# Kernel optimization log

Measured on AMD Instinct MI355X. Metric: run time of the kernel, lower is better.

Reference implementation:

```python
import jax, jax.numpy as jnp
import numpy as np

NUM_HEADS = 16
NUM_UNITS = 1024
NEG = -2.0**32 + 1.0
EPS = 1e-8


def setup_inputs() -> dict:
    key = jax.random.key(0)
    ks = jax.random.split(key, 8)
    B, T, C = 2, 2048, 1024
    U = NUM_UNITS
    x = jax.random.normal(ks[0], (B, T, C), dtype=jnp.float32)
    s = 1.0 / np.sqrt(C)
    Wq = jax.random.normal(ks[1], (C, U), dtype=jnp.float32) * s
    Wk = jax.random.normal(ks[2], (C, U), dtype=jnp.float32) * s
    Wv = jax.random.normal(ks[3], (C, U), dtype=jnp.float32) * s
    bq = jnp.zeros((U,), dtype=jnp.float32)
    bk = jnp.zeros((U,), dtype=jnp.float32)
    bv = jnp.zeros((U,), dtype=jnp.float32)
    gamma = jnp.ones((U,), dtype=jnp.float32)
    beta = jnp.zeros((U,), dtype=jnp.float32)
    return {"x": x, "Wq": Wq, "bq": bq, "Wk": Wk, "bk": bk,
            "Wv": Wv, "bv": bv, "gamma": gamma, "beta": beta}


def _attention(x, Wq, bq, Wk, bk, Wv, bv, gamma, beta):
    B, T, C = x.shape
    H = NUM_HEADS
    U = NUM_UNITS
    dh = U // H
    # Dense projections with relu activation (Keras Dense(activation='relu'))
    Q = jax.nn.relu(x @ Wq + bq)  # [B, T, U]
    K = jax.nn.relu(x @ Wk + bk)
    V = jax.nn.relu(x @ Wv + bv)
    # split into heads: tf.split(axis=2) + concat(axis=0) == [B, T, H, dh]
    Qh = Q.reshape(B, T, H, dh)
    Kh = K.reshape(B, T, H, dh)
    Vh = V.reshape(B, T, H, dh)
    # scaled dot-product scores: scale by sqrt(d_head) (K_ last dim after split)
    scores = jnp.einsum('bqhd,bkhd->bhqk', Qh, Kh) / np.sqrt(dh)
    # key mask: sign(|sum(keys, -1)|) over the ORIGINAL keys input (= x)
    key_mask = jnp.sign(jnp.abs(jnp.sum(x, axis=-1)))  # [B, Tk]
    scores = jnp.where(key_mask[:, None, None, :] == 0, NEG, scores)
    # causal mask (lower-triangular)
    tril = jnp.tril(jnp.ones((T, T), dtype=scores.dtype))
    scores = jnp.where(tril[None, None, :, :] == 0, NEG, scores)
    attn = jax.nn.softmax(scores, axis=-1)
    # query mask: multiply attention rows for zero queries
    query_mask = jnp.sign(jnp.abs(jnp.sum(x, axis=-1)))  # [B, Tq]
    attn = attn * query_mask[:, None, :, None]
    # dropout rate is 0 -> identity
    out = jnp.einsum('bhqk,bkhd->bqhd', attn, Vh).reshape(B, T, U)
    # residual with original queries
    out = out + x
    # layer norm over last axis (tf.nn.moments: biased variance)
    mean = jnp.mean(out, axis=-1, keepdims=True)
    var = jnp.mean((out - mean) ** 2, axis=-1, keepdims=True)
    normalized = (out - mean) / jnp.sqrt(var + EPS)
    return gamma * normalized + beta


def reference(x, Wq, bq, Wk, bk, Wv, bv, gamma, beta):
    return _attention(x, Wq, bq, Wk, bk, Wv, bv, gamma, beta)
```

## Files before the change

kernel.cpp:

```cpp
#include <hip/hip_runtime.h>
#include <math.h>

#define BB 2
#define TT 2048
#define CC 1024
#define UU 1024
#define HH 16
#define DH 64
#define BT (BB*TT)

typedef __attribute__((ext_vector_type(8))) __bf16 bf16x8;
typedef __attribute__((ext_vector_type(4))) __bf16 bf16x4;
typedef __attribute__((ext_vector_type(4))) float f32x4;

#define GLL16(g, l) __builtin_amdgcn_global_load_lds( \
    (__attribute__((address_space(1))) const void*)(g), \
    (__attribute__((address_space(3))) void*)(l), 16, 0, 0)

#define C2EXP 0.18033688011112042f
#define MBIAS 64.0f

__global__ __launch_bounds__(256) void prep_kernel(
    const float* __restrict__ x, float* __restrict__ kadd, __bf16* __restrict__ xb,
    const float* __restrict__ Wq, const float* __restrict__ Wk,
    const float* __restrict__ Wv, __bf16* __restrict__ Wt) {
    const int bx = blockIdx.x;
    const int t = threadIdx.x;
    if (bx < BT) {
        int row = bx;
        float4 v = *(const float4*)&x[(size_t)row * CC + t * 4];
        bf16x4 o;
        o[0] = (__bf16)v.x; o[1] = (__bf16)v.y; o[2] = (__bf16)v.z; o[3] = (__bf16)v.w;
        *(bf16x4*)&xb[(size_t)row * CC + t * 4] = o;
        float s = v.x + v.y + v.z + v.w;
#pragma unroll
        for (int off = 32; off; off >>= 1) s += __shfl_down(s, off, 64);
        __shared__ float red[4];
        int lane = t & 63, w = t >> 6;
        if (lane == 0) red[w] = s;
        __syncthreads();
        if (t == 0) {
            float tot = red[0] + red[1] + red[2] + red[3];
            kadd[row] = (tot == 0.f ? -1.0e30f : 0.f) - MBIAS;
        }
    } else {
        int bz = bx - BT;
        int z = bz >> 8, rem = bz & 255;
        const float* W = z == 0 ? Wq : (z == 1 ? Wk : Wv);
        __bf16* Out = Wt + (size_t)z * CC * UU;
        __shared__ float tile[64][65];
        int n0 = (rem & 15) * 64, k0 = (rem >> 4) * 64;
        int r = t >> 4, c4 = (t & 15) * 4;
#pragma unroll
        for (int i = 0; i < 4; ++i) {
            float4 v = *(const float4*)&W[(size_t)(k0 + r + i * 16) * UU + n0 + c4];
            tile[r + i * 16][c4 + 0] = v.x; tile[r + i * 16][c4 + 1] = v.y;
            tile[r + i * 16][c4 + 2] = v.z; tile[r + i * 16][c4 + 3] = v.w;
        }
        __syncthreads();
#pragma unroll
        for (int i = 0; i < 4; ++i) {
            int nr = r + i * 16;
            bf16x4 o;
            o[0] = (__bf16)tile[c4 + 0][nr]; o[1] = (__bf16)tile[c4 + 1][nr];
            o[2] = (__bf16)tile[c4 + 2][nr]; o[3] = (__bf16)tile[c4 + 3][nr];
            *(bf16x4*)&Out[(size_t)(n0 + nr) * CC + k0 + c4] = o;
        }
    }
}

__global__ __launch_bounds__(256, 4) void qkv_mfma(
    const __bf16* __restrict__ xb, const __bf16* __restrict__ Wt_all,
    const float* __restrict__ bq, const float* __restrict__ bk,
    const float* __restrict__ bv,
    __bf16* __restrict__ Qo, __bf16* __restrict__ Ko, __bf16* __restrict__ VTo) {
    const int z = blockIdx.z;
    const __bf16* Wt = Wt_all + (size_t)z * CC * UU;
    const float* bias = z == 0 ? bq : (z == 1 ? bk : bv);

    const int n0 = blockIdx.x * 128, m0 = blockIdx.y * 128;
    const int t = threadIdx.x, w = t >> 6, lane = t & 63;
    const int quad = lane >> 4, nn = lane & 15;
    const int wr = w >> 1, wc = w & 1;

    __shared__ __bf16 smem[2 * 128 * 64];
    __bf16* As = smem;
    __bf16* Bs = smem + 128 * 64;

    f32x4 acc[4][4];
#pragma unroll
    for (int i = 0; i < 4; ++i)
#pragma unroll
        for (int j = 0; j < 4; ++j) acc[i][j] = (f32x4){0.f, 0.f, 0.f, 0.f};

    for (int k0 = 0; k0 < CC; k0 += 64) {
        __syncthreads();
#pragma unroll
        for (int i = 0; i < 4; ++i) {
            int c = i * 256 + t;
            int row = c >> 3;
            int gc = ((c & 7) ^ (row & 7)) * 8;
            GLL16(&xb[(size_t)(m0 + row) * CC + k0 + gc], &As[c * 8]);
            GLL16(&Wt[(size_t)(n0 + row) * CC + k0 + gc], &Bs[c * 8]);
        }
        __syncthreads();
#pragma unroll
        for (int kk = 0; kk < 2; ++kk) {
            bf16x8 af[4], bfr[4];
#pragma unroll
            for (int i = 0; i < 4; ++i) {
                int R = wr * 64 + i * 16 + nn;
                af[i] = *(const bf16x8*)&As[R * 64 + (((kk * 4 + quad) ^ (R & 7)) * 8)];
            }
#pragma unroll
            for (int j = 0; j < 4; ++j) {
                int R = wc * 64 + j * 16 + nn;
                bfr[j] = *(const bf16x8*)&Bs[R * 64 + (((kk * 4 + quad) ^ (R & 7)) * 8)];
            }
#pragma unroll
            for (int i = 0; i < 4; ++i)
#pragma unroll
                for (int j = 0; j < 4; ++j)
                    acc[i][j] = __builtin_amdgcn_mfma_f32_16x16x32_bf16(af[i], bfr[j], acc[i][j], 0, 0, 0);
        }
    }

    __bf16* cw = &smem[w * 1024];
    float bv4[4];
#pragma unroll
    for (int j = 0; j < 4; ++j) bv4[j] = bias[n0 + wc * 64 + j * 16 + nn];

    if (z < 2) {
        __bf16* Out = z == 0 ? Qo : Ko;
#pragma unroll
        for (int i = 0; i < 4; ++i) {
            __syncthreads();
#pragma unroll
            for (int j = 0; j < 4; ++j)
#pragma unroll
                for (int r = 0; r < 4; ++r)
                    cw[(quad * 4 + r) * 64 + j * 16 + nn] =
                        (__bf16)fmaxf(acc[i][j][r] + bv4[j], 0.f);
            __syncthreads();
            int rr = lane >> 2, cc = (lane & 3) * 16;
            bf16x8 v0 = *(const bf16x8*)&cw[rr * 64 + cc];
            bf16x8 v1 = *(const bf16x8*)&cw[rr * 64 + cc + 8];
            size_t o = (size_t)(m0 + wr * 64 + i * 16 + rr) * UU + n0 + wc * 64 + cc;
            *(bf16x8*)&Out[o] = v0;
            *(bf16x8*)&Out[o + 8] = v1;
        }
    } else {
#pragma unroll
        for (int i = 0; i < 4; ++i) {
            __syncthreads();
#pragma unroll
            for (int j = 0; j < 4; ++j)
#pragma unroll
                for (int r = 0; r < 4; ++r)
                    cw[(j * 16 + nn) * 16 + quad * 4 + r] =
                        (__bf16)fmaxf(acc[i][j][r] + bv4[j], 0.f);
            __syncthreads();
            bf16x8 v0 = *(const bf16x8*)&cw[lane * 16];
            bf16x8 v1 = *(const bf16x8*)&cw[lane * 16 + 8];
            size_t o = (size_t)(n0 + wc * 64 + lane) * BT + m0 + wr * 64 + i * 16;
            *(bf16x8*)&VTo[o] = v0;
            *(bf16x8*)&VTo[o + 8] = v1;
        }
    }
}

__global__ __launch_bounds__(256, 4) void attn_mfma(
    const __bf16* __restrict__ Q, const __bf16* __restrict__ K,
    const __bf16* __restrict__ Vt, const float* __restrict__ kadd,
    float* __restrict__ Op0, float* __restrict__ Op1,
    float* __restrict__ lq0, float* __restrict__ lq1) {
    const int cx = blockIdx.x;
    const int bh = blockIdx.y, b = bh >> 4, h = bh & 15;
    int qt, kst, ket, slot;
    if (cx < 16) { qt = cx; kst = 0; ket = qt; slot = 0; }
    else {
        int q2 = (cx - 16) >> 1;
        qt = 16 + q2;
        int len0 = (qt + 2) >> 1;
        slot = (cx - 16) & 1;
        if (slot) { kst = len0; ket = qt; }
        else      { kst = 0;    ket = len0 - 1; }
    }
    const int col0 = h * 64, rowbase = b * TT, q0 = qt * 64;
    const bool hasdiag = (ket == qt);

    const int t = threadIdx.x;
    const int w = t >> 6, lane = t & 63, quad = lane >> 4, nn = lane & 15;
    const int s7 = nn & 7;

    __shared__ __align__(16) __bf16 ks[2][64 * 64];
    __shared__ __align__(16) __bf16 vt[2][64 * 64];
    __shared__ __align__(16) __bf16 ps[64 * 64];

    const int c0 = t;
    const int r0 = c0 >> 3, g0 = ((c0 & 7) ^ (r0 & 7)) * 8;
    const int prow = 16 * w + nn;
    const int qg = q0 + prow;

    const __bf16* kp0 = &K[(size_t)(rowbase + kst * 64 + r0) * UU + col0 + g0];
    const __bf16* kp1 = kp0 + 32 * (size_t)UU;
    const __bf16* vp0 = &Vt[(size_t)(col0 + r0) * BT + rowbase + kst * 64 + g0];
    const __bf16* vp1 = vp0 + 32 * (size_t)BT;
    const float* kap = &kadd[rowbase + kst * 64 + quad * 4];

    f32x4 ka[4];
#pragma unroll
    for (int ct = 0; ct < 4; ++ct) ka[ct] = *(const f32x4*)&kap[ct * 16];
    kap += 64;
    const __bf16* qrow = &Q[(size_t)(rowbase + qg) * UU + col0];
    bf16x8 bq0 = *(const bf16x8*)&qrow[quad * 8];
    bf16x8 bq1 = *(const bf16x8*)&qrow[32 + quad * 8];

    GLL16(kp0, &ks[0][c0 * 8]);
    GLL16(kp1, &ks[0][c0 * 8 + 2048]);
    GLL16(vp0, &vt[0][c0 * 8]);
    GLL16(vp1, &vt[0][c0 * 8 + 2048]);
    kp0 += 64 * (size_t)UU; kp1 += 64 * (size_t)UU;
    vp0 += 64; vp1 += 64;
    asm volatile("s_waitcnt vmcnt(0)" ::: "memory");
    __builtin_amdgcn_s_barrier();

    float lp = 0.f;
    f32x4 oc[4];
#pragma unroll
    for (int dt = 0; dt < 4; ++dt) oc[dt] = (f32x4){0.f, 0.f, 0.f, 0.f};

#define ATTN_CORE(KSC, VTC, DIAG)                                              \
  {                                                                            \
    const __bf16* ksc = (KSC);                                                 \
    const __bf16* vtc = (VTC);                                                 \
    _Pragma("unroll")                                                          \
    for (int ct = 0; ct < 4; ++ct) {                                           \
      int krow = ct * 16 + nn;                                                 \
      bf16x8 a0 = *(const bf16x8*)&ksc[krow * 64 + ((quad ^ s7) * 8)];         \
      bf16x8 a1 = *(const bf16x8*)&ksc[krow * 64 + (((4 + quad) ^ s7) * 8)];   \
      f32x4 sc = (f32x4){0.f, 0.f, 0.f, 0.f};                                  \
      sc = __builtin_amdgcn_mfma_f32_16x16x32_bf16(a0, bq0, sc, 0, 0, 0);      \
      sc = __builtin_amdgcn_mfma_f32_16x16x32_bf16(a1, bq1, sc, 0, 0, 0);      \
      bf16x4 pw;                                                               \
      _Pragma("unroll")                                                        \
      for (int r = 0; r < 4; ++r) {                                            \
        float arg = fmaf(sc[r], C2EXP, ka[ct][r]);                             \
        if (DIAG) {                                                            \
          int kl = ct * 16 + quad * 4 + r;                                     \
          if (kl > prow) arg = -1.0e30f;                                       \
        }                                                                      \
        float p = __builtin_amdgcn_exp2f(arg);                                 \
        lp += p;                                                               \
        pw[r] = (__bf16)p;                                                     \
      }                                                                        \
      int chunk = ct * 2 + (quad >> 1);                                        \
      *(bf16x4*)&ps[prow * 64 + ((chunk ^ s7) * 8) + (quad & 1) * 4] = pw;     \
    }                                                                          \
    bf16x8 bp0 = *(const bf16x8*)&ps[prow * 64 + ((quad ^ s7) * 8)];           \
    bf16x8 bp1 = *(const bf16x8*)&ps[prow * 64 + (((4 + quad) ^ s7) * 8)];     \
    _Pragma("unroll")                                                          \
    for (int dt = 0; dt < 4; ++dt) {                                           \
      int vrow = dt * 16 + nn;                                                 \
      bf16x8 a0 = *(const bf16x8*)&vtc[vrow * 64 + ((quad ^ s7) * 8)];         \
      bf16x8 a1 = *(const bf16x8*)&vtc[vrow * 64 + (((4 + quad) ^ s7) * 8)];   \
      oc[dt] = __builtin_amdgcn_mfma_f32_16x16x32_bf16(a0, bp0, oc[dt], 0, 0, 0); \
      oc[dt] = __builtin_amdgcn_mfma_f32_16x16x32_bf16(a1, bp1, oc[dt], 0, 0, 0); \
    }                                                                          \
  }

    int cur = 0;
    for (int kt = kst; kt < ket; ++kt) {
        f32x4 kan[4];
#pragma unroll
        for (int ct = 0; ct < 4; ++ct) kan[ct] = *(const f32x4*)&kap[ct * 16];
        kap += 64;
        GLL16(kp0, &ks[cur ^ 1][c0 * 8]);
        GLL16(kp1, &ks[cur ^ 1][c0 * 8 + 2048]);
        GLL16(vp0, &vt[cur ^ 1][c0 * 8]);
        GLL16(vp1, &vt[cur ^ 1][c0 * 8 + 2048]);
        kp0 += 64 * (size_t)UU; kp1 += 64 * (size_t)UU;
        vp0 += 64; vp1 += 64;
        ATTN_CORE(ks[cur], vt[cur], false)
#pragma unroll
        for (int ct = 0; ct < 4; ++ct) ka[ct] = kan[ct];
        cur ^= 1;
        asm volatile("s_waitcnt vmcnt(0)" ::: "memory");
        __builtin_amdgcn_s_barrier();
    }
    if (hasdiag) {
        ATTN_CORE(ks[cur], vt[cur], true)
    } else {
        ATTN_CORE(ks[cur], vt[cur], false)
    }
#undef ATTN_CORE

    float l = lp;
    l += __shfl_xor(l, 16, 64);
    l += __shfl_xor(l, 32, 64);
    const int grow = rowbase + qg;
    float* Op;
    size_t orow;
    if (slot) { Op = Op1; orow = (size_t)(grow - (b + 1) * 1024); }
    else      { Op = Op0; orow = (size_t)grow; }
    if (quad == 0) (slot ? lq1 : lq0)[(size_t)grow * HH + h] = l;
#pragma unroll
    for (int dt = 0; dt < 4; ++dt)
        *(f32x4*)&Op[orow * UU + col0 + dt * 16 + quad * 4] = oc[dt];
}

__global__ __launch_bounds__(256) void ln_kernel(
    const float* __restrict__ Op0, const float* __restrict__ Op1,
    const float* __restrict__ lq0, const float* __restrict__ lq1,
    const float* __restrict__ kadd, const float* __restrict__ x,
    const float* __restrict__ gamma, const float* __restrict__ beta,
    float* __restrict__ out) {
    int row = blockIdx.x;
    int b = row >> 11;
    int qt = (row & (TT - 1)) >> 6;
    size_t base = (size_t)row * UU;
    int t = threadIdx.x;
    int h = t >> 4;
    float l = lq0[(size_t)row * HH + h];
    f32x4 o = *(const f32x4*)&Op0[base + t * 4];
    if (qt >= 16) {
        l += lq1[(size_t)row * HH + h];
        size_t base1 = (size_t)(row - (b + 1) * 1024) * UU;
        f32x4 o1 = *(const f32x4*)&Op1[base1 + t * 4];
        o[0] += o1[0]; o[1] += o1[1]; o[2] += o1[2]; o[3] += o1[3];
    }
    float qsel = (kadd[row] < -1.0e29f) ? 0.f : 1.f;
    float mult = qsel / fmaxf(l, 1e-37f);
    float4 xv = *(const float4*)&x[base + t * 4];
    float v0 = o[0] * mult + xv.x, v1 = o[1] * mult + xv.y;
    float v2 = o[2] * mult + xv.z, v3 = o[3] * mult + xv.w;
    float s1 = v0 + v1 + v2 + v3;
    float s2 = v0 * v0 + v1 * v1 + v2 * v2 + v3 * v3;
#pragma unroll
    for (int off = 32; off; off >>= 1) {
        s1 += __shfl_down(s1, off, 64);
        s2 += __shfl_down(s2, off, 64);
    }
    __shared__ float r1[4], r2[4];
    int lane = t & 63, w = t >> 6;
    if (lane == 0) { r1[w] = s1; r2[w] = s2; }
    __syncthreads();
    s1 = r1[0] + r1[1] + r1[2] + r1[3];
    s2 = r2[0] + r2[1] + r2[2] + r2[3];
    float mean = s1 * (1.0f / 1024.0f);
    float var = s2 * (1.0f / 1024.0f) - mean * mean;
    float rstd = rsqrtf(var + 1e-8f);
    float4 g = *(const float4*)&gamma[t * 4];
    float4 be = *(const float4*)&beta[t * 4];
    float4 ores;
    ores.x = g.x * (v0 - mean) * rstd + be.x;
    ores.y = g.y * (v1 - mean) * rstd + be.y;
    ores.z = g.z * (v2 - mean) * rstd + be.z;
    ores.w = g.w * (v3 - mean) * rstd + be.w;
    *(float4*)&out[base + t * 4] = ores;
}

extern "C" void kernel_launch(void* const* d_in, const int* in_sizes, int n_in,
                              void* d_out, int out_size, void* d_ws, size_t ws_size,
                              hipStream_t stream) {
    const float* x     = (const float*)d_in[0];
    const float* Wq    = (const float*)d_in[1];
    const float* bq    = (const float*)d_in[2];
    const float* Wk    = (const float*)d_in[3];
    const float* bk    = (const float*)d_in[4];
    const float* Wv    = (const float*)d_in[5];
    const float* bv    = (const float*)d_in[6];
    const float* gamma = (const float*)d_in[7];
    const float* beta  = (const float*)d_in[8];
    float* out = (float*)d_out;

    char* wsb = (char*)d_ws;
    const size_t MB = 1024ull * 1024;
    __bf16* xb = (__bf16*)(wsb);
    __bf16* Wt = (__bf16*)(wsb + 8 * MB);
    float* Op0 = (float*)(wsb);
    __bf16* Qb = (__bf16*)(wsb + 16 * MB);
    __bf16* Kb = (__bf16*)(wsb + 24 * MB);
    __bf16* Vt = (__bf16*)(wsb + 32 * MB);
    float* kadd = (float*)(wsb + 40 * MB);
    float* Op1  = (float*)(wsb + 41 * MB);
    float* lq0  = (float*)(wsb + 49 * MB);
    float* lq1  = (float*)(wsb + 50 * MB);

    prep_kernel<<<dim3(BT + 768), dim3(256), 0, stream>>>(x, kadd, xb, Wq, Wk, Wv, Wt);
    qkv_mfma<<<dim3(UU / 128, BT / 128, 3), dim3(256), 0, stream>>>(
        xb, Wt, bq, bk, bv, Qb, Kb, Vt);
    attn_mfma<<<dim3(48, BB * HH), dim3(256), 0, stream>>>(
        Qb, Kb, Vt, kadd, Op0, Op1, lq0, lq1);
    ln_kernel<<<dim3(BT), dim3(256), 0, stream>>>(
        Op0, Op1, lq0, lq1, kadd, x, gamma, beta, out);
}
```

Before: 180.6 us.

## Pair light and heavy causal query tiles per block for balanced attention work

Changes the causal attention work split. Before, each block took one query tile, and the longer tiles were split in two. Now each of 32 blocks per head pairs query tile p with tile 31-p, with the two halves of the key range covering the pair's combined work, so every block does about 17 key tiles. The short tiles are finished in place and written already normalized as bf16, which lets the layer-norm kernel skip reading partial sums and row totals for those rows. The cost is a more complex control flow with a shared LDS double buffer carried across the two tiles, and reduced precision in the stored attention output for half the rows.

```diff
diff --git a/kernel.cpp b/kernel.cpp
--- a/kernel.cpp
+++ b/kernel.cpp
@@ -172,22 +172,13 @@
 __global__ __launch_bounds__(256, 4) void attn_mfma(
     const __bf16* __restrict__ Q, const __bf16* __restrict__ K,
     const __bf16* __restrict__ Vt, const float* __restrict__ kadd,
-    float* __restrict__ Op0, float* __restrict__ Op1,
+    __bf16* __restrict__ Obf, float* __restrict__ Op0, float* __restrict__ Op1,
     float* __restrict__ lq0, float* __restrict__ lq1) {
     const int cx = blockIdx.x;
+    const int p = cx >> 1, half = cx & 1;
     const int bh = blockIdx.y, b = bh >> 4, h = bh & 15;
-    int qt, kst, ket, slot;
-    if (cx < 16) { qt = cx; kst = 0; ket = qt; slot = 0; }
-    else {
-        int q2 = (cx - 16) >> 1;
-        qt = 16 + q2;
-        int len0 = (qt + 2) >> 1;
-        slot = (cx - 16) & 1;
-        if (slot) { kst = len0; ket = qt; }
-        else      { kst = 0;    ket = len0 - 1; }
-    }
-    const int col0 = h * 64, rowbase = b * TT, q0 = qt * 64;
-    const bool hasdiag = (ket == qt);
+    const int col0 = h * 64, rowbase = b * TT;
+    const int qa = p, qb = 31 - p;
 
     const int t = threadIdx.x;
     const int w = t >> 6, lane = t & 63, quad = lane >> 4, nn = lane & 15;
@@ -200,35 +191,27 @@
     const int c0 = t;
     const int r0 = c0 >> 3, g0 = ((c0 & 7) ^ (r0 & 7)) * 8;
     const int prow = 16 * w + nn;
-    const int qg = q0 + prow;
-
-    const __bf16* kp0 = &K[(size_t)(rowbase + kst * 64 + r0) * UU + col0 + g0];
-    const __bf16* kp1 = kp0 + 32 * (size_t)UU;
-    const __bf16* vp0 = &Vt[(size_t)(col0 + r0) * BT + rowbase + kst * 64 + g0];
-    const __bf16* vp1 = vp0 + 32 * (size_t)BT;
-    const float* kap = &kadd[rowbase + kst * 64 + quad * 4];
-
-    f32x4 ka[4];
-#pragma unroll
-    for (int ct = 0; ct < 4; ++ct) ka[ct] = *(const f32x4*)&kap[ct * 16];
-    kap += 64;
-    const __bf16* qrow = &Q[(size_t)(rowbase + qg) * UU + col0];
-    bf16x8 bq0 = *(const bf16x8*)&qrow[quad * 8];
-    bf16x8 bq1 = *(const bf16x8*)&qrow[32 + quad * 8];
-
-    GLL16(kp0, &ks[0][c0 * 8]);
-    GLL16(kp1, &ks[0][c0 * 8 + 2048]);
-    GLL16(vp0, &vt[0][c0 * 8]);
-    GLL16(vp1, &vt[0][c0 * 8 + 2048]);
-    kp0 += 64 * (size_t)UU; kp1 += 64 * (size_t)UU;
-    vp0 += 64; vp1 += 64;
-    asm volatile("s_waitcnt vmcnt(0)" ::: "memory");
-    __builtin_amdgcn_s_barrier();
+
+    const size_t KSTRIDE = 64 * (size_t)UU;
+    const __bf16* kb0 = &K[(size_t)(rowbase + r0) * UU + col0 + g0];
+    const __bf16* kb1 = kb0 + 32 * (size_t)UU;
+    const __bf16* vb0 = &Vt[(size_t)(col0 + r0) * BT + rowbase + g0];
+    const __bf16* vb1 = vb0 + 32 * (size_t)BT;
+    const float* kab = &kadd[rowbase + quad * 4];
+
+#define STAGE_TILE(BUF, KP0, KP1, VP0, VP1)   \
+    GLL16((KP0), &ks[BUF][c0 * 8]);           \
+    GLL16((KP1), &ks[BUF][c0 * 8 + 2048]);    \
+    GLL16((VP0), &vt[BUF][c0 * 8]);           \
+    GLL16((VP1), &vt[BUF][c0 * 8 + 2048]);
 
     float lp = 0.f;
     f32x4 oc[4];
 #pragma unroll
     for (int dt = 0; dt < 4; ++dt) oc[dt] = (f32x4){0.f, 0.f, 0.f, 0.f};
+    int cur = 0;
+    f32x4 ka[4];
+    bf16x8 bq0, bq1;
 
 #define ATTN_CORE(KSC, VTC, DIAG)                                              \
   {                                                                            \
@@ -250,11 +233,11 @@
           int kl = ct * 16 + quad * 4 + r;                                     \
           if (kl > prow) arg = -1.0e30f;                                       \
         }                                                                      \
-        float p = __builtin_amdgcn_exp2f(arg);                                 \
-        lp += p;                                                               \
-        pw[r] = (__bf16)p;                                                     \
+        float pv = __builtin_amdgcn_exp2f(arg);                                \
+        lp += pv;                                                              \
+        pw[r] = (__bf16)pv;                                                    \
       }                                                                        \
-      int chunk = ct * 2 + (quad >> 1);                                        \
+      int chunk = ct * 2 + (quad >> 1);                                       \
       *(bf16x4*)&ps[prow * 64 + ((chunk ^ s7) * 8) + (quad & 1) * 4] = pw;     \
     }                                                                          \
     bf16x8 bp0 = *(const bf16x8*)&ps[prow * 64 + ((quad ^ s7) * 8)];           \
@@ -269,71 +252,176 @@
     }                                                                          \
   }
 
-    int cur = 0;
-    for (int kt = kst; kt < ket; ++kt) {
-        f32x4 kan[4];
-#pragma unroll
-        for (int ct = 0; ct < 4; ++ct) kan[ct] = *(const f32x4*)&kap[ct * 16];
-        kap += 64;
-        GLL16(kp0, &ks[cur ^ 1][c0 * 8]);
-        GLL16(kp1, &ks[cur ^ 1][c0 * 8 + 2048]);
-        GLL16(vp0, &vt[cur ^ 1][c0 * 8]);
-        GLL16(vp1, &vt[cur ^ 1][c0 * 8 + 2048]);
-        kp0 += 64 * (size_t)UU; kp1 += 64 * (size_t)UU;
-        vp0 += 64; vp1 += 64;
-        ATTN_CORE(ks[cur], vt[cur], false)
-#pragma unroll
-        for (int ct = 0; ct < 4; ++ct) ka[ct] = kan[ct];
-        cur ^= 1;
+    if (half == 0) {
+#pragma unroll
+        for (int ct = 0; ct < 4; ++ct) ka[ct] = *(const f32x4*)&kab[ct * 16];
+        {
+            const __bf16* qrow = &Q[(size_t)(rowbase + qa * 64 + prow) * UU + col0];
+            bq0 = *(const bf16x8*)&qrow[quad * 8];
+            bq1 = *(const bf16x8*)&qrow[32 + quad * 8];
+        }
+        const __bf16* kp0 = kb0; const __bf16* kp1 = kb1;
+        const __bf16* vp0 = vb0; const __bf16* vp1 = vb1;
+        STAGE_TILE(0, kp0, kp1, vp0, vp1)
+        kp0 += KSTRIDE; kp1 += KSTRIDE; vp0 += 64; vp1 += 64;
         asm volatile("s_waitcnt vmcnt(0)" ::: "memory");
         __builtin_amdgcn_s_barrier();
-    }
-    if (hasdiag) {
+
+        for (int kt = 0; kt < qa; ++kt) {
+            f32x4 kan[4];
+#pragma unroll
+            for (int ct = 0; ct < 4; ++ct)
+                kan[ct] = *(const f32x4*)&kab[(kt + 1) * 64 + ct * 16];
+            STAGE_TILE(cur ^ 1, kp0, kp1, vp0, vp1)
+            kp0 += KSTRIDE; kp1 += KSTRIDE; vp0 += 64; vp1 += 64;
+            ATTN_CORE(ks[cur], vt[cur], false)
+#pragma unroll
+            for (int ct = 0; ct < 4; ++ct) ka[ct] = kan[ct];
+            cur ^= 1;
+            asm volatile("s_waitcnt vmcnt(0)" ::: "memory");
+            __builtin_amdgcn_s_barrier();
+        }
+        {
+            f32x4 kan[4];
+#pragma unroll
+            for (int ct = 0; ct < 4; ++ct) kan[ct] = *(const f32x4*)&kab[ct * 16];
+            STAGE_TILE(cur ^ 1, kb0, kb1, vb0, vb1)
+            ATTN_CORE(ks[cur], vt[cur], true)
+#pragma unroll
+            for (int ct = 0; ct < 4; ++ct) ka[ct] = kan[ct];
+            cur ^= 1;
+            asm volatile("s_waitcnt vmcnt(0)" ::: "memory");
+            __builtin_amdgcn_s_barrier();
+        }
+        {
+            float l = lp;
+            l += __shfl_xor(l, 16, 64);
+            l += __shfl_xor(l, 32, 64);
+            const int grow = rowbase + qa * 64 + prow;
+            float qsel = (kadd[grow] < -1.0e29f) ? 0.f : 1.f;
+            float mult = qsel / fmaxf(l, 1e-37f);
+#pragma unroll
+            for (int dt = 0; dt < 4; ++dt) {
+                bf16x4 ov;
+                ov[0] = (__bf16)(oc[dt][0] * mult); ov[1] = (__bf16)(oc[dt][1] * mult);
+                ov[2] = (__bf16)(oc[dt][2] * mult); ov[3] = (__bf16)(oc[dt][3] * mult);
+                *(bf16x4*)&Obf[(size_t)grow * UU + col0 + dt * 16 + quad * 4] = ov;
+            }
+        }
+        lp = 0.f;
+#pragma unroll
+        for (int dt = 0; dt < 4; ++dt) oc[dt] = (f32x4){0.f, 0.f, 0.f, 0.f};
+        {
+            const __bf16* qrow = &Q[(size_t)(rowbase + qb * 64 + prow) * UU + col0];
+            bq0 = *(const bf16x8*)&qrow[quad * 8];
+            bq1 = *(const bf16x8*)&qrow[32 + quad * 8];
+        }
+        kp0 = kb0 + KSTRIDE; kp1 = kb1 + KSTRIDE; vp0 = vb0 + 64; vp1 = vb1 + 64;
+        const int nb = 16 - p;
+        for (int kt = 0; kt < nb - 1; ++kt) {
+            f32x4 kan[4];
+#pragma unroll
+            for (int ct = 0; ct < 4; ++ct)
+                kan[ct] = *(const f32x4*)&kab[(kt + 1) * 64 + ct * 16];
+            STAGE_TILE(cur ^ 1, kp0, kp1, vp0, vp1)
+            kp0 += KSTRIDE; kp1 += KSTRIDE; vp0 += 64; vp1 += 64;
+            ATTN_CORE(ks[cur], vt[cur], false)
+#pragma unroll
+            for (int ct = 0; ct < 4; ++ct) ka[ct] = kan[ct];
+            cur ^= 1;
+            asm volatile("s_waitcnt vmcnt(0)" ::: "memory");
+            __builtin_amdgcn_s_barrier();
+        }
+        ATTN_CORE(ks[cur], vt[cur], false)
+        {
+            float l = lp;
+            l += __shfl_xor(l, 16, 64);
+            l += __shfl_xor(l, 32, 64);
+            const int grow = rowbase + qb * 64 + prow;
+            if (quad == 0) lq0[(size_t)grow * HH + h] = l;
+            size_t orow = (size_t)(grow - (b + 1) * 1024);
+#pragma unroll
+            for (int dt = 0; dt < 4; ++dt)
+                *(f32x4*)&Op0[orow * UU + col0 + dt * 16 + quad * 4] = oc[dt];
+        }
+    } else {
+        const int k0t = 16 - p;
+#pragma unroll
+        for (int ct = 0; ct < 4; ++ct)
+            ka[ct] = *(const f32x4*)&kab[k0t * 64 + ct * 16];
+        {
+            const __bf16* qrow = &Q[(size_t)(rowbase + qb * 64 + prow) * UU + col0];
+            bq0 = *(const bf16x8*)&qrow[quad * 8];
+            bq1 = *(const bf16x8*)&qrow[32 + quad * 8];
+        }
+        const __bf16* kp0 = kb0 + (size_t)k0t * KSTRIDE;
+        const __bf16* kp1 = kb1 + (size_t)k0t * KSTRIDE;
+        const __bf16* vp0 = vb0 + k0t * 64;
+        const __bf16* vp1 = vb1 + k0t * 64;
+        STAGE_TILE(0, kp0, kp1, vp0, vp1)
+        kp0 += KSTRIDE; kp1 += KSTRIDE; vp0 += 64; vp1 += 64;
+        asm volatile("s_waitcnt vmcnt(0)" ::: "memory");
+        __builtin_amdgcn_s_barrier();
+
+        for (int i = 0; i < 15; ++i) {
+            f32x4 kan[4];
+#pragma unroll
+            for (int ct = 0; ct < 4; ++ct)
+                kan[ct] = *(const f32x4*)&kab[(k0t + i + 1) * 64 + ct * 16];
+            STAGE_TILE(cur ^ 1, kp0, kp1, vp0, vp1)
+            kp0 += KSTRIDE; kp1 += KSTRIDE; vp0 += 64; vp1 += 64;
+            ATTN_CORE(ks[cur], vt[cur], false)
+#pragma unroll
+            for (int ct = 0; ct < 4; ++ct) ka[ct] = kan[ct];
+            cur ^= 1;
+            asm volatile("s_waitcnt vmcnt(0)" ::: "memory");
+            __builtin_amdgcn_s_barrier();
+        }
         ATTN_CORE(ks[cur], vt[cur], true)
-    } else {
-        ATTN_CORE(ks[cur], vt[cur], false)
+        {
+            float l = lp;
+            l += __shfl_xor(l, 16, 64);
+            l += __shfl_xor(l, 32, 64);
+            const int grow = rowbase + qb * 64 + prow;
+            if (quad == 0) lq1[(size_t)grow * HH + h] = l;
+            size_t orow = (size_t)(grow - (b + 1) * 1024);
+#pragma unroll
+            for (int dt = 0; dt < 4; ++dt)
+                *(f32x4*)&Op1[orow * UU + col0 + dt * 16 + quad * 4] = oc[dt];
+        }
     }
 #undef ATTN_CORE
-
-    float l = lp;
-    l += __shfl_xor(l, 16, 64);
-    l += __shfl_xor(l, 32, 64);
-    const int grow = rowbase + qg;
-    float* Op;
-    size_t orow;
-    if (slot) { Op = Op1; orow = (size_t)(grow - (b + 1) * 1024); }
-    else      { Op = Op0; orow = (size_t)grow; }
-    if (quad == 0) (slot ? lq1 : lq0)[(size_t)grow * HH + h] = l;
-#pragma unroll
-    for (int dt = 0; dt < 4; ++dt)
-        *(f32x4*)&Op[orow * UU + col0 + dt * 16 + quad * 4] = oc[dt];
+#undef STAGE_TILE
 }
 
 __global__ __launch_bounds__(256) void ln_kernel(
-    const float* __restrict__ Op0, const float* __restrict__ Op1,
-    const float* __restrict__ lq0, const float* __restrict__ lq1,
-    const float* __restrict__ kadd, const float* __restrict__ x,
-    const float* __restrict__ gamma, const float* __restrict__ beta,
-    float* __restrict__ out) {
+    const __bf16* __restrict__ Obf, const float* __restrict__ Op0,
+    const float* __restrict__ Op1, const float* __restrict__ lq0,
+    const float* __restrict__ lq1, const float* __restrict__ kadd,
+    const float* __restrict__ x, const float* __restrict__ gamma,
+    const float* __restrict__ beta, float* __restrict__ out) {
     int row = blockIdx.x;
     int b = row >> 11;
     int qt = (row & (TT - 1)) >> 6;
     size_t base = (size_t)row * UU;
     int t = threadIdx.x;
-    int h = t >> 4;
-    float l = lq0[(size_t)row * HH + h];
-    f32x4 o = *(const f32x4*)&Op0[base + t * 4];
-    if (qt >= 16) {
-        l += lq1[(size_t)row * HH + h];
+    float v0, v1, v2, v3;
+    float4 xv = *(const float4*)&x[base + t * 4];
+    if (qt < 16) {
+        bf16x4 ov = *(const bf16x4*)&Obf[base + t * 4];
+        v0 = (float)ov[0] + xv.x; v1 = (float)ov[1] + xv.y;
+        v2 = (float)ov[2] + xv.z; v3 = (float)ov[3] + xv.w;
+    } else {
+        int h = t >> 4;
+        float l = lq0[(size_t)row * HH + h] + lq1[(size_t)row * HH + h];
         size_t base1 = (size_t)(row - (b + 1) * 1024) * UU;
+        f32x4 o0 = *(const f32x4*)&Op0[base1 + t * 4];
         f32x4 o1 = *(const f32x4*)&Op1[base1 + t * 4];
-        o[0] += o1[0]; o[1] += o1[1]; o[2] += o1[2]; o[3] += o1[3];
-    }
-    float qsel = (kadd[row] < -1.0e29f) ? 0.f : 1.f;
-    float mult = qsel / fmaxf(l, 1e-37f);
-    float4 xv = *(const float4*)&x[base + t * 4];
-    float v0 = o[0] * mult + xv.x, v1 = o[1] * mult + xv.y;
-    float v2 = o[2] * mult + xv.z, v3 = o[3] * mult + xv.w;
+        float qsel = (kadd[row] < -1.0e29f) ? 0.f : 1.f;
+        float mult = qsel / fmaxf(l, 1e-37f);
+        v0 = (o0[0] + o1[0]) * mult + xv.x; v1 = (o0[1] + o1[1]) * mult + xv.y;
+        v2 = (o0[2] + o1[2]) * mult + xv.z; v3 = (o0[3] + o1[3]) * mult + xv.w;
+    }
     float s1 = v0 + v1 + v2 + v3;
     float s2 = v0 * v0 + v1 * v1 + v2 * v2 + v3 * v3;
 #pragma unroll
@@ -376,12 +464,13 @@
 
     char* wsb = (char*)d_ws;
     const size_t MB = 1024ull * 1024;
-    __bf16* xb = (__bf16*)(wsb);
-    __bf16* Wt = (__bf16*)(wsb + 8 * MB);
-    float* Op0 = (float*)(wsb);
-    __bf16* Qb = (__bf16*)(wsb + 16 * MB);
-    __bf16* Kb = (__bf16*)(wsb + 24 * MB);
-    __bf16* Vt = (__bf16*)(wsb + 32 * MB);
+    __bf16* xb  = (__bf16*)(wsb);
+    __bf16* Wt  = (__bf16*)(wsb + 8 * MB);
+    __bf16* Obf = (__bf16*)(wsb);
+    float* Op0  = (float*)(wsb + 8 * MB);
+    __bf16* Qb  = (__bf16*)(wsb + 16 * MB);
+    __bf16* Kb  = (__bf16*)(wsb + 24 * MB);
+    __bf16* Vt  = (__bf16*)(wsb + 32 * MB);
     float* kadd = (float*)(wsb + 40 * MB);
     float* Op1  = (float*)(wsb + 41 * MB);
     float* lq0  = (float*)(wsb + 49 * MB);
@@ -390,8 +479,8 @@
     prep_kernel<<<dim3(BT + 768), dim3(256), 0, stream>>>(x, kadd, xb, Wq, Wk, Wv, Wt);
     qkv_mfma<<<dim3(UU / 128, BT / 128, 3), dim3(256), 0, stream>>>(
         xb, Wt, bq, bk, bv, Qb, Kb, Vt);
-    attn_mfma<<<dim3(48, BB * HH), dim3(256), 0, stream>>>(
-        Qb, Kb, Vt, kadd, Op0, Op1, lq0, lq1);
+    attn_mfma<<<dim3(32, BB * HH), dim3(256), 0, stream>>>(
+        Qb, Kb, Vt, kadd, Obf, Op0, Op1, lq0, lq1);
     ln_kernel<<<dim3(BT), dim3(256), 0, stream>>>(
-        Op0, Op1, lq0, lq1, kadd, x, gamma, beta, out);
+        Obf, Op0, Op1, lq0, lq1, kadd, x, gamma, beta, out);
 }
```

New measurement: 170.9 us. -5.4%, faster.
